# Kernel tuning notes

Measured on AMD Instinct MI355X. Metric: run time of the kernel, lower is better.

## Reference

```python
import jax, jax.numpy as jnp
import numpy as np


def setup_inputs() -> dict:
    key = jax.random.key(0)
    k1, k2, k3, k4 = jax.random.split(key, 4)
    B, C, N, K, OUT = 2, 64, 50000, 9, 64
    x = jax.random.normal(k1, (B, C, N, 1), dtype=jnp.float32)
    edge_index = jax.random.randint(k2, (2, B, N, K), 0, N, dtype=jnp.int64)
    W1 = jax.random.normal(k3, (C, C), dtype=jnp.float32) * (1.0 / np.sqrt(C))
    b1 = jnp.zeros((C,), dtype=jnp.float32)
    W2 = jax.random.normal(k4, (OUT, 2 * C), dtype=jnp.float32) * (1.0 / np.sqrt(2 * C))
    b2 = jnp.zeros((OUT,), dtype=jnp.float32)
    return {"x": x, "edge_index": edge_index, "W1": W1, "b1": b1, "W2": W2, "b2": b2}


def _gather_neighbors(x_sq, idx):
    # x_sq: [B, C, N], idx: [B, N, K] -> [B, C, N, K]
    B, C, N = x_sq.shape
    K = idx.shape[-1]
    flat = jax.vmap(lambda xb, ib: xb[:, ib])(x_sq, idx.reshape(B, N * K))
    return flat.reshape(B, C, N, K)


def reference(x, edge_index, W1, b1, W2, b2):
    # x: [B, C, N, 1]; edge_index[0]: [B, N, K] neighbor indices
    x_sq = x[..., 0]                                   # [B, C, N]
    x_j = _gather_neighbors(x_sq, edge_index[0])       # [B, C, N, K]
    # nn1: 1x1 conv (per-node linear over channels) + ReLU
    h = jax.nn.relu(jnp.einsum('bcnk,dc->bdnk', x_j, W1) + b1[None, :, None, None])
    x_j_max = jnp.max(h, axis=-1, keepdims=True)       # [B, C, N, 1]
    cat = jnp.concatenate([x, x_j_max], axis=1)        # [B, 2C, N, 1]
    # nn2: 1x1 conv + ReLU
    out = jax.nn.relu(jnp.einsum('bcnk,dc->bdnk', cat, W2) + b2[None, :, None, None])
    return out                                          # [B, OUT, N, 1]
```

## Files before the change

### kernel.cpp

```cpp
#include <hip/hip_runtime.h>
#include <cstddef>

typedef unsigned int uint;
typedef _Float16 half2v __attribute__((ext_vector_type(2)));
typedef __fp16 fp16v2 __attribute__((ext_vector_type(2)));
typedef unsigned short us2v __attribute__((ext_vector_type(2)));

union U32H2 { uint u; half2v h; fp16v2 g; us2v s; };

__device__ __forceinline__ uint pkh2(float a, float b) {
  U32H2 v; v.g = __builtin_amdgcn_cvt_pkrtz(a, b); return v.u;
}
__device__ __forceinline__ uint hmax2u(uint a, uint b) {
  U32H2 x, y, r; x.u = a; y.u = b;
  r.s = __builtin_elementwise_max(x.s, y.s);
  return r.u;
}
__device__ __forceinline__ float fdot2(uint wa, uint xa, float acc) {
  U32H2 w, x; w.u = wa; x.u = xa;
#if __has_builtin(__builtin_amdgcn_fdot2)
  return __builtin_amdgcn_fdot2(w.h, x.h, acc, false);
#else
  return acc + (float)w.h[0] * (float)x.h[0] + (float)w.h[1] * (float)x.h[1];
#endif
}

__global__ __launch_bounds__(256) void k1_node_mlp(
    const float* __restrict__ x, const float* __restrict__ W1,
    const float* __restrict__ b1, unsigned short* __restrict__ y, int N)
{
  __shared__ __align__(16) uint xs2[32 * 64];
  __shared__ __align__(16) uint wt2[32 * 64];
  const int t = threadIdx.x;
  const int nblk = (N + 63) >> 6;
  const int b = blockIdx.x / nblk;
  const int n0 = (blockIdx.x % nblk) << 6;

#pragma unroll
  for (int it = 0; it < 8; ++it) {
    const int i = t + (it << 8);
    const int n = i & 63, c2 = i >> 6;
    const bool valid = (n0 + n) < N;
    const float* xp = x + (size_t)b * 64 * N + n0 + n;
    const float a = valid ? xp[(size_t)(2 * c2) * N] : 0.0f;
    const float c = valid ? xp[(size_t)(2 * c2 + 1) * N] : 0.0f;
    xs2[c2 * 64 + n] = pkh2(a, c);
  }
#pragma unroll
  for (int it = 0; it < 8; ++it) {
    const int i = t + (it << 8);
    const int d = i & 63, c2 = i >> 6;
    wt2[c2 * 64 + d] = pkh2(W1[d * 64 + 2 * c2], W1[d * 64 + 2 * c2 + 1]);
  }
  __syncthreads();

  const int n_off = (t & 15) << 2;
  const int d0 = (t >> 4) << 2;
  float acc[4][4];
#pragma unroll
  for (int i = 0; i < 4; ++i) {
    const float bv = b1[d0 + i];
#pragma unroll
    for (int j = 0; j < 4; ++j) acc[i][j] = bv;
  }
#pragma unroll 8
  for (int c2 = 0; c2 < 32; ++c2) {
    const uint4 w = *(const uint4*)(wt2 + c2 * 64 + d0);
    const uint4 xv = *(const uint4*)(xs2 + c2 * 64 + n_off);
    const uint wa[4] = {w.x, w.y, w.z, w.w};
    const uint xa[4] = {xv.x, xv.y, xv.z, xv.w};
#pragma unroll
    for (int i = 0; i < 4; ++i)
#pragma unroll
      for (int j = 0; j < 4; ++j)
        acc[i][j] = fdot2(wa[i], xa[j], acc[i][j]);
  }
#pragma unroll
  for (int j = 0; j < 4; ++j) {
    const int n = n0 + n_off + j;
    if (n < N) {
      uint2 v;
      v.x = pkh2(fmaxf(acc[0][j], 0.f), fmaxf(acc[1][j], 0.f));
      v.y = pkh2(fmaxf(acc[2][j], 0.f), fmaxf(acc[3][j], 0.f));
      *(uint2*)(y + ((size_t)b * N + n) * 64 + d0) = v;
    }
  }
}

__global__ __launch_bounds__(256, 4) void k2_gather_out(
    const float* __restrict__ x, const int* __restrict__ eidx,
    const unsigned short* __restrict__ y, const float* __restrict__ W2,
    const float* __restrict__ b2, float* __restrict__ out, int N, int K)
{
  __shared__ __align__(16) uint ins2[64 * 64];
  __shared__ __align__(16) uint wt2[64 * 64];
  const int t = threadIdx.x;
  const int nblk = (N + 63) >> 6;
  const int b = blockIdx.x / nblk;
  const int n0 = (blockIdx.x % nblk) << 6;

  const int lane = t & 63;
  const bool is64 = (__ballot(eidx[2 * lane + 1] == 0) == ~0ull);

  const int node = lane;
  const int seg = t >> 6;
  const int n = n0 + node;
  int jj[9];
  bool act = (n < N) && (K == 9);
  if (act) {
    const size_t r = (size_t)b * N + n;
    if (is64) {
      const uint2* p = (const uint2*)(eidx + r * 18);
#pragma unroll
      for (int k = 0; k < 9; ++k) jj[k] = (int)p[k].x;
    } else {
      const int* p = eidx + r * 9;
#pragma unroll
      for (int k = 0; k < 9; ++k) jj[k] = p[k];
    }
  }

#pragma unroll
  for (int it = 0; it < 8; ++it) {
    const int i = t + (it << 8);
    const int nn = i & 63, c2 = i >> 6;
    const bool valid = (n0 + nn) < N;
    const float* xp = x + (size_t)b * 64 * N + n0 + nn;
    const float a = valid ? xp[(size_t)(2 * c2) * N] : 0.0f;
    const float c = valid ? xp[(size_t)(2 * c2 + 1) * N] : 0.0f;
    ins2[c2 * 64 + nn] = pkh2(a, c);
  }
#pragma unroll
  for (int it = 0; it < 16; ++it) {
    const int i = t + (it << 8);
    const int o = i & 63, c2 = i >> 6;
    wt2[c2 * 64 + o] = pkh2(W2[o * 128 + 2 * c2], W2[o * 128 + 2 * c2 + 1]);
  }

  uint m[8] = {0, 0, 0, 0, 0, 0, 0, 0};
  if (act) {
    const unsigned short* yb = y + (size_t)b * N * 64 + seg * 16;
    uint4 g[18];
#pragma unroll
    for (int k = 0; k < 9; ++k) {
      const uint4* yr = (const uint4*)(yb + (size_t)jj[k] * 64);
      g[2 * k] = yr[0];
      g[2 * k + 1] = yr[1];
    }
#pragma unroll
    for (int k = 0; k < 9; ++k) {
      m[0] = hmax2u(m[0], g[2 * k].x);
      m[1] = hmax2u(m[1], g[2 * k].y);
      m[2] = hmax2u(m[2], g[2 * k].z);
      m[3] = hmax2u(m[3], g[2 * k].w);
      m[4] = hmax2u(m[4], g[2 * k + 1].x);
      m[5] = hmax2u(m[5], g[2 * k + 1].y);
      m[6] = hmax2u(m[6], g[2 * k + 1].z);
      m[7] = hmax2u(m[7], g[2 * k + 1].w);
    }
  } else if (n < N) {
    const size_t r = (size_t)b * N + n;
    const unsigned short* yb = y + (size_t)b * N * 64 + seg * 16;
    for (int k = 0; k < K; ++k) {
      const int j = is64 ? (int)((const uint2*)(eidx + r * 2 * K))[k].x
                         : (eidx + r * K)[k];
      const uint4* yr = (const uint4*)(yb + (size_t)j * 64);
      const uint4 a0 = yr[0], a1 = yr[1];
      m[0] = hmax2u(m[0], a0.x); m[1] = hmax2u(m[1], a0.y);
      m[2] = hmax2u(m[2], a0.z); m[3] = hmax2u(m[3], a0.w);
      m[4] = hmax2u(m[4], a1.x); m[5] = hmax2u(m[5], a1.y);
      m[6] = hmax2u(m[6], a1.z); m[7] = hmax2u(m[7], a1.w);
    }
  }
#pragma unroll
  for (int q = 0; q < 8; ++q)
    ins2[(32 + seg * 8 + q) * 64 + node] = m[q];
  __syncthreads();

  const int n_off = (t & 15) << 2;
  const int o0 = (t >> 4) << 2;
  float acc[4][4];
#pragma unroll
  for (int i = 0; i < 4; ++i) {
    const float bv = b2[o0 + i];
#pragma unroll
    for (int j = 0; j < 4; ++j) acc[i][j] = bv;
  }
#pragma unroll 8
  for (int c2 = 0; c2 < 64; ++c2) {
    const uint4 w = *(const uint4*)(wt2 + c2 * 64 + o0);
    const uint4 xv = *(const uint4*)(ins2 + c2 * 64 + n_off);
    const uint wa[4] = {w.x, w.y, w.z, w.w};
    const uint xa[4] = {xv.x, xv.y, xv.z, xv.w};
#pragma unroll
    for (int i = 0; i < 4; ++i)
#pragma unroll
      for (int j = 0; j < 4; ++j)
        acc[i][j] = fdot2(wa[i], xa[j], acc[i][j]);
  }
#pragma unroll
  for (int i = 0; i < 4; ++i) {
    const int o = o0 + i;
    float* op = out + (size_t)(b * 64 + o) * N + n0 + n_off;
    const float4 v = make_float4(fmaxf(acc[i][0], 0.f), fmaxf(acc[i][1], 0.f),
                                 fmaxf(acc[i][2], 0.f), fmaxf(acc[i][3], 0.f));
    if (n0 + n_off + 3 < N) {
      *(float4*)op = v;
    } else {
      const float va[4] = {v.x, v.y, v.z, v.w};
      for (int j = 0; j < 4; ++j)
        if (n0 + n_off + j < N) op[j] = va[j];
    }
  }
}

extern "C" void kernel_launch(void* const* d_in, const int* in_sizes, int n_in,
                              void* d_out, int out_size, void* d_ws, size_t ws_size,
                              hipStream_t stream) {
  const float* x  = (const float*)d_in[0];
  const int*   ei = (const int*)d_in[1];
  const float* W1 = (const float*)d_in[2];
  const float* b1 = (const float*)d_in[3];
  const float* W2 = (const float*)d_in[4];
  const float* b2 = (const float*)d_in[5];
  float* out = (float*)d_out;

  const int N = in_sizes[0] / 128;
  const int K = in_sizes[1] / (4 * N);

  unsigned short* y = (unsigned short*)d_ws;

  const int nblk = (N + 63) >> 6;
  k1_node_mlp<<<2 * nblk, 256, 0, stream>>>(x, W1, b1, y, N);
  k2_gather_out<<<2 * nblk, 256, 0, stream>>>(x, ei, y, W2, b2, out, N, K);
}
```

Measured before the change: 144.9 us.

## Use MFMA 16x16x32 f16 for both node linears with node-major LDS layout

Both per-node linear layers move from scalar fdot2 register-tile GEMMs to MFMA 16x16x32 f16 instructions. Weight fragments are loaded straight from global memory into registers instead of being staged in LDS, and activations are stored node-major with padded strides. Each thread in k2 now handles one quarter of one node's channels for the neighbor max, with the 9 gathers split into batches of 5 and 4 to limit register use. Outputs are written as scalar per-channel stores, which may coalesce worse than the previous float4 stores.

```diff
diff --git a/kernel.cpp b/kernel.cpp
--- a/kernel.cpp
+++ b/kernel.cpp
@@ -2,11 +2,13 @@
 #include <cstddef>
 
 typedef unsigned int uint;
-typedef _Float16 half2v __attribute__((ext_vector_type(2)));
+typedef _Float16 v8h __attribute__((ext_vector_type(8)));
+typedef float v4f __attribute__((ext_vector_type(4)));
 typedef __fp16 fp16v2 __attribute__((ext_vector_type(2)));
 typedef unsigned short us2v __attribute__((ext_vector_type(2)));
 
-union U32H2 { uint u; half2v h; fp16v2 g; us2v s; };
+union U32H2 { uint u; fp16v2 g; us2v s; };
+union Frag8 { uint4 u4; uint u[4]; v8h h; };
 
 __device__ __forceinline__ uint pkh2(float a, float b) {
   U32H2 v; v.g = __builtin_amdgcn_cvt_pkrtz(a, b); return v.u;
@@ -16,101 +18,121 @@
   r.s = __builtin_elementwise_max(x.s, y.s);
   return r.u;
 }
-__device__ __forceinline__ float fdot2(uint wa, uint xa, float acc) {
-  U32H2 w, x; w.u = wa; x.u = xa;
-#if __has_builtin(__builtin_amdgcn_fdot2)
-  return __builtin_amdgcn_fdot2(w.h, x.h, acc, false);
-#else
-  return acc + (float)w.h[0] * (float)x.h[0] + (float)w.h[1] * (float)x.h[1];
-#endif
-}
-
-__global__ __launch_bounds__(256) void k1_node_mlp(
+
+__global__ __launch_bounds__(256, 4) void k1_node_mlp(
     const float* __restrict__ x, const float* __restrict__ W1,
-    const float* __restrict__ b1, unsigned short* __restrict__ y, int N)
+    const float* __restrict__ b1, uint* __restrict__ y, int N)
 {
-  __shared__ __align__(16) uint xs2[32 * 64];
-  __shared__ __align__(16) uint wt2[32 * 64];
+  __shared__ __align__(16) uint xlds[64 * 36];
+  __shared__ __align__(16) uint ylds[64 * 34];
   const int t = threadIdx.x;
   const int nblk = (N + 63) >> 6;
   const int b = blockIdx.x / nblk;
   const int n0 = (blockIdx.x % nblk) << 6;
-
-#pragma unroll
-  for (int it = 0; it < 8; ++it) {
-    const int i = t + (it << 8);
-    const int n = i & 63, c2 = i >> 6;
-    const bool valid = (n0 + n) < N;
-    const float* xp = x + (size_t)b * 64 * N + n0 + n;
-    const float a = valid ? xp[(size_t)(2 * c2) * N] : 0.0f;
-    const float c = valid ? xp[(size_t)(2 * c2 + 1) * N] : 0.0f;
-    xs2[c2 * 64 + n] = pkh2(a, c);
-  }
-#pragma unroll
-  for (int it = 0; it < 8; ++it) {
-    const int i = t + (it << 8);
-    const int d = i & 63, c2 = i >> 6;
-    wt2[c2 * 64 + d] = pkh2(W1[d * 64 + 2 * c2], W1[d * 64 + 2 * c2 + 1]);
+  const int lane = t & 63;
+  const int w = t >> 6;
+  const int node = t >> 2;
+  const int cg = t & 3;
+
+  {
+    const bool valid = (n0 + node) < N;
+    const float* xp = x + (size_t)b * 64 * N + n0 + node;
+    float xv[16];
+#pragma unroll
+    for (int i = 0; i < 16; ++i)
+      xv[i] = valid ? xp[(size_t)(cg * 16 + i) * N] : 0.0f;
+    uint4 p0, p1;
+    p0.x = pkh2(xv[0], xv[1]);   p0.y = pkh2(xv[2], xv[3]);
+    p0.z = pkh2(xv[4], xv[5]);   p0.w = pkh2(xv[6], xv[7]);
+    p1.x = pkh2(xv[8], xv[9]);   p1.y = pkh2(xv[10], xv[11]);
+    p1.z = pkh2(xv[12], xv[13]); p1.w = pkh2(xv[14], xv[15]);
+    uint* dst = xlds + node * 36 + cg * 8;
+    *(uint4*)dst = p0;
+    *(uint4*)(dst + 4) = p1;
+  }
+
+  Frag8 af[2];
+  {
+    const int d_row = w * 16 + (lane & 15);
+    const int kb = (lane >> 4) * 8;
+    const float* wp = W1 + d_row * 64 + kb;
+#pragma unroll
+    for (int kk = 0; kk < 2; ++kk) {
+      const float4 fa = *(const float4*)(wp + kk * 32);
+      const float4 fb = *(const float4*)(wp + kk * 32 + 4);
+      af[kk].u4.x = pkh2(fa.x, fa.y);
+      af[kk].u4.y = pkh2(fa.z, fa.w);
+      af[kk].u4.z = pkh2(fb.x, fb.y);
+      af[kk].u4.w = pkh2(fb.z, fb.w);
+    }
   }
   __syncthreads();
 
-  const int n_off = (t & 15) << 2;
-  const int d0 = (t >> 4) << 2;
-  float acc[4][4];
-#pragma unroll
-  for (int i = 0; i < 4; ++i) {
-    const float bv = b1[d0 + i];
-#pragma unroll
-    for (int j = 0; j < 4; ++j) acc[i][j] = bv;
-  }
-#pragma unroll 8
-  for (int c2 = 0; c2 < 32; ++c2) {
-    const uint4 w = *(const uint4*)(wt2 + c2 * 64 + d0);
-    const uint4 xv = *(const uint4*)(xs2 + c2 * 64 + n_off);
-    const uint wa[4] = {w.x, w.y, w.z, w.w};
-    const uint xa[4] = {xv.x, xv.y, xv.z, xv.w};
-#pragma unroll
-    for (int i = 0; i < 4; ++i)
-#pragma unroll
-      for (int j = 0; j < 4; ++j)
-        acc[i][j] = fdot2(wa[i], xa[j], acc[i][j]);
-  }
-#pragma unroll
-  for (int j = 0; j < 4; ++j) {
-    const int n = n0 + n_off + j;
-    if (n < N) {
-      uint2 v;
-      v.x = pkh2(fmaxf(acc[0][j], 0.f), fmaxf(acc[1][j], 0.f));
-      v.y = pkh2(fmaxf(acc[2][j], 0.f), fmaxf(acc[3][j], 0.f));
-      *(uint2*)(y + ((size_t)b * N + n) * 64 + d0) = v;
+  const int q = lane >> 4;
+  const int cidx = lane & 15;
+  const int d0 = w * 16;
+  v4f acc[4];
+  {
+    v4f bi;
+#pragma unroll
+    for (int r = 0; r < 4; ++r) bi[r] = b1[d0 + q * 4 + r];
+#pragma unroll
+    for (int nt = 0; nt < 4; ++nt) acc[nt] = bi;
+  }
+#pragma unroll
+  for (int nt = 0; nt < 4; ++nt) {
+#pragma unroll
+    for (int kk = 0; kk < 2; ++kk) {
+      Frag8 bf;
+      bf.u4 = *(const uint4*)(xlds + (nt * 16 + cidx) * 36 + kk * 16 + q * 4);
+      acc[nt] = __builtin_amdgcn_mfma_f32_16x16x32_f16(af[kk].h, bf.h, acc[nt], 0, 0, 0);
+    }
+  }
+
+#pragma unroll
+  for (int nt = 0; nt < 4; ++nt) {
+    const int nn = nt * 16 + cidx;
+    const uint p01 = pkh2(fmaxf(acc[nt][0], 0.f), fmaxf(acc[nt][1], 0.f));
+    const uint p23 = pkh2(fmaxf(acc[nt][2], 0.f), fmaxf(acc[nt][3], 0.f));
+    ylds[nn * 34 + (d0 >> 1) + 2 * q] = p01;
+    ylds[nn * 34 + (d0 >> 1) + 2 * q + 1] = p23;
+  }
+  __syncthreads();
+#pragma unroll
+  for (int p = 0; p < 4; ++p) {
+    const int f = t + (p << 8);
+    const int nn = f >> 4, ch = f & 15;
+    if (n0 + nn < N) {
+      const uint2 v = *(const uint2*)(ylds + nn * 34 + ch * 2);
+      *(uint2*)(y + ((size_t)b * N + n0 + nn) * 32 + ch * 2) = v;
     }
   }
 }
 
 __global__ __launch_bounds__(256, 4) void k2_gather_out(
     const float* __restrict__ x, const int* __restrict__ eidx,
-    const unsigned short* __restrict__ y, const float* __restrict__ W2,
+    const uint* __restrict__ y, const float* __restrict__ W2,
     const float* __restrict__ b2, float* __restrict__ out, int N, int K)
 {
-  __shared__ __align__(16) uint ins2[64 * 64];
-  __shared__ __align__(16) uint wt2[64 * 64];
+  __shared__ __align__(16) uint blds[64 * 68];
   const int t = threadIdx.x;
   const int nblk = (N + 63) >> 6;
   const int b = blockIdx.x / nblk;
   const int n0 = (blockIdx.x % nblk) << 6;
-
   const int lane = t & 63;
+  const int w = t >> 6;
+  const int node = t >> 2;
+  const int cg = t & 3;
+  const int n = n0 + node;
+
   const bool is64 = (__ballot(eidx[2 * lane + 1] == 0) == ~0ull);
 
-  const int node = lane;
-  const int seg = t >> 6;
-  const int n = n0 + node;
   int jj[9];
-  bool act = (n < N) && (K == 9);
+  const bool act = (n < N) && (K == 9);
   if (act) {
     const size_t r = (size_t)b * N + n;
     if (is64) {
-      const uint2* p = (const uint2*)(eidx + r * 18);
+      const uint2* p = (const uint2*)eidx + r * 9;
 #pragma unroll
       for (int k = 0; k < 9; ++k) jj[k] = (int)p[k].x;
     } else {
@@ -120,96 +142,122 @@
     }
   }
 
-#pragma unroll
-  for (int it = 0; it < 8; ++it) {
-    const int i = t + (it << 8);
-    const int nn = i & 63, c2 = i >> 6;
-    const bool valid = (n0 + nn) < N;
-    const float* xp = x + (size_t)b * 64 * N + n0 + nn;
-    const float a = valid ? xp[(size_t)(2 * c2) * N] : 0.0f;
-    const float c = valid ? xp[(size_t)(2 * c2 + 1) * N] : 0.0f;
-    ins2[c2 * 64 + nn] = pkh2(a, c);
-  }
-#pragma unroll
-  for (int it = 0; it < 16; ++it) {
-    const int i = t + (it << 8);
-    const int o = i & 63, c2 = i >> 6;
-    wt2[c2 * 64 + o] = pkh2(W2[o * 128 + 2 * c2], W2[o * 128 + 2 * c2 + 1]);
+  {
+    const bool valid = n < N;
+    const float* xp = x + (size_t)b * 64 * N + n0 + node;
+    float xv[16];
+#pragma unroll
+    for (int i = 0; i < 16; ++i)
+      xv[i] = valid ? xp[(size_t)(cg * 16 + i) * N] : 0.0f;
+    uint4 p0, p1;
+    p0.x = pkh2(xv[0], xv[1]);   p0.y = pkh2(xv[2], xv[3]);
+    p0.z = pkh2(xv[4], xv[5]);   p0.w = pkh2(xv[6], xv[7]);
+    p1.x = pkh2(xv[8], xv[9]);   p1.y = pkh2(xv[10], xv[11]);
+    p1.z = pkh2(xv[12], xv[13]); p1.w = pkh2(xv[14], xv[15]);
+    uint* dst = blds + node * 68 + cg * 8;
+    *(uint4*)dst = p0;
+    *(uint4*)(dst + 4) = p1;
+  }
+
+  Frag8 af[4];
+  {
+    const int o_row = w * 16 + (lane & 15);
+    const int kb = (lane >> 4) * 8;
+    const float* wp = W2 + o_row * 128 + kb;
+#pragma unroll
+    for (int kk = 0; kk < 4; ++kk) {
+      const float4 fa = *(const float4*)(wp + kk * 32);
+      const float4 fb = *(const float4*)(wp + kk * 32 + 4);
+      af[kk].u4.x = pkh2(fa.x, fa.y);
+      af[kk].u4.y = pkh2(fa.z, fa.w);
+      af[kk].u4.z = pkh2(fb.x, fb.y);
+      af[kk].u4.w = pkh2(fb.z, fb.w);
+    }
   }
 
   uint m[8] = {0, 0, 0, 0, 0, 0, 0, 0};
   if (act) {
-    const unsigned short* yb = y + (size_t)b * N * 64 + seg * 16;
-    uint4 g[18];
-#pragma unroll
-    for (int k = 0; k < 9; ++k) {
-      const uint4* yr = (const uint4*)(yb + (size_t)jj[k] * 64);
-      g[2 * k] = yr[0];
-      g[2 * k + 1] = yr[1];
-    }
-#pragma unroll
-    for (int k = 0; k < 9; ++k) {
-      m[0] = hmax2u(m[0], g[2 * k].x);
-      m[1] = hmax2u(m[1], g[2 * k].y);
-      m[2] = hmax2u(m[2], g[2 * k].z);
-      m[3] = hmax2u(m[3], g[2 * k].w);
-      m[4] = hmax2u(m[4], g[2 * k + 1].x);
-      m[5] = hmax2u(m[5], g[2 * k + 1].y);
-      m[6] = hmax2u(m[6], g[2 * k + 1].z);
-      m[7] = hmax2u(m[7], g[2 * k + 1].w);
+    const uint* yb = y + (size_t)b * N * 32 + cg * 8;
+    uint4 g[10];
+#pragma unroll
+    for (int k = 0; k < 5; ++k) {
+      const uint* base = yb + (size_t)jj[k] * 32;
+      g[2 * k] = *(const uint4*)base;
+      g[2 * k + 1] = *(const uint4*)(base + 4);
+    }
+#pragma unroll
+    for (int k = 0; k < 5; ++k) {
+      m[0] = hmax2u(m[0], g[2 * k].x); m[1] = hmax2u(m[1], g[2 * k].y);
+      m[2] = hmax2u(m[2], g[2 * k].z); m[3] = hmax2u(m[3], g[2 * k].w);
+      m[4] = hmax2u(m[4], g[2 * k + 1].x); m[5] = hmax2u(m[5], g[2 * k + 1].y);
+      m[6] = hmax2u(m[6], g[2 * k + 1].z); m[7] = hmax2u(m[7], g[2 * k + 1].w);
+    }
+#pragma unroll
+    for (int k = 0; k < 4; ++k) {
+      const uint* base = yb + (size_t)jj[5 + k] * 32;
+      g[2 * k] = *(const uint4*)base;
+      g[2 * k + 1] = *(const uint4*)(base + 4);
+    }
+#pragma unroll
+    for (int k = 0; k < 4; ++k) {
+      m[0] = hmax2u(m[0], g[2 * k].x); m[1] = hmax2u(m[1], g[2 * k].y);
+      m[2] = hmax2u(m[2], g[2 * k].z); m[3] = hmax2u(m[3], g[2 * k].w);
+      m[4] = hmax2u(m[4], g[2 * k + 1].x); m[5] = hmax2u(m[5], g[2 * k + 1].y);
+      m[6] = hmax2u(m[6], g[2 * k + 1].z); m[7] = hmax2u(m[7], g[2 * k + 1].w);
     }
   } else if (n < N) {
     const size_t r = (size_t)b * N + n;
-    const unsigned short* yb = y + (size_t)b * N * 64 + seg * 16;
+    const uint* yb = y + (size_t)b * N * 32 + cg * 8;
     for (int k = 0; k < K; ++k) {
-      const int j = is64 ? (int)((const uint2*)(eidx + r * 2 * K))[k].x
+      const int j = is64 ? (int)((const uint2*)eidx + r * K)[k].x
                          : (eidx + r * K)[k];
-      const uint4* yr = (const uint4*)(yb + (size_t)j * 64);
-      const uint4 a0 = yr[0], a1 = yr[1];
+      const uint* base = yb + (size_t)j * 32;
+      const uint4 a0 = *(const uint4*)base, a1 = *(const uint4*)(base + 4);
       m[0] = hmax2u(m[0], a0.x); m[1] = hmax2u(m[1], a0.y);
       m[2] = hmax2u(m[2], a0.z); m[3] = hmax2u(m[3], a0.w);
       m[4] = hmax2u(m[4], a1.x); m[5] = hmax2u(m[5], a1.y);
       m[6] = hmax2u(m[6], a1.z); m[7] = hmax2u(m[7], a1.w);
     }
   }
-#pragma unroll
-  for (int q = 0; q < 8; ++q)
-    ins2[(32 + seg * 8 + q) * 64 + node] = m[q];
+  {
+    uint* dst = blds + node * 68 + 32 + cg * 8;
+    uint4 v0; v0.x = m[0]; v0.y = m[1]; v0.z = m[2]; v0.w = m[3];
+    uint4 v1; v1.x = m[4]; v1.y = m[5]; v1.z = m[6]; v1.w = m[7];
+    *(uint4*)dst = v0;
+    *(uint4*)(dst + 4) = v1;
+  }
   __syncthreads();
 
-  const int n_off = (t & 15) << 2;
-  const int o0 = (t >> 4) << 2;
-  float acc[4][4];
-#pragma unroll
-  for (int i = 0; i < 4; ++i) {
-    const float bv = b2[o0 + i];
-#pragma unroll
-    for (int j = 0; j < 4; ++j) acc[i][j] = bv;
-  }
-#pragma unroll 8
-  for (int c2 = 0; c2 < 64; ++c2) {
-    const uint4 w = *(const uint4*)(wt2 + c2 * 64 + o0);
-    const uint4 xv = *(const uint4*)(ins2 + c2 * 64 + n_off);
-    const uint wa[4] = {w.x, w.y, w.z, w.w};
-    const uint xa[4] = {xv.x, xv.y, xv.z, xv.w};
-#pragma unroll
-    for (int i = 0; i < 4; ++i)
-#pragma unroll
-      for (int j = 0; j < 4; ++j)
-        acc[i][j] = fdot2(wa[i], xa[j], acc[i][j]);
-  }
-#pragma unroll
-  for (int i = 0; i < 4; ++i) {
-    const int o = o0 + i;
-    float* op = out + (size_t)(b * 64 + o) * N + n0 + n_off;
-    const float4 v = make_float4(fmaxf(acc[i][0], 0.f), fmaxf(acc[i][1], 0.f),
-                                 fmaxf(acc[i][2], 0.f), fmaxf(acc[i][3], 0.f));
-    if (n0 + n_off + 3 < N) {
-      *(float4*)op = v;
-    } else {
-      const float va[4] = {v.x, v.y, v.z, v.w};
-      for (int j = 0; j < 4; ++j)
-        if (n0 + n_off + j < N) op[j] = va[j];
+  const int q = lane >> 4;
+  const int cidx = lane & 15;
+  const int o0 = w * 16;
+  v4f acc[4];
+  {
+    v4f bi;
+#pragma unroll
+    for (int r = 0; r < 4; ++r) bi[r] = b2[o0 + q * 4 + r];
+#pragma unroll
+    for (int nt = 0; nt < 4; ++nt) acc[nt] = bi;
+  }
+#pragma unroll
+  for (int nt = 0; nt < 4; ++nt) {
+#pragma unroll
+    for (int kk = 0; kk < 4; ++kk) {
+      Frag8 bf;
+      bf.u4 = *(const uint4*)(blds + (nt * 16 + cidx) * 68 + kk * 16 + q * 4);
+      acc[nt] = __builtin_amdgcn_mfma_f32_16x16x32_f16(af[kk].h, bf.h, acc[nt], 0, 0, 0);
+    }
+  }
+
+#pragma unroll
+  for (int nt = 0; nt < 4; ++nt) {
+    const int nn = n0 + nt * 16 + cidx;
+    if (nn < N) {
+#pragma unroll
+      for (int r = 0; r < 4; ++r) {
+        const int o = o0 + q * 4 + r;
+        out[(size_t)(b * 64 + o) * N + nn] = fmaxf(acc[nt][r], 0.f);
+      }
     }
   }
 }
@@ -228,7 +276,7 @@
   const int N = in_sizes[0] / 128;
   const int K = in_sizes[1] / (4 * N);
 
-  unsigned short* y = (unsigned short*)d_ws;
+  uint* y = (uint*)d_ws;
 
   const int nblk = (N + 63) >> 6;
   k1_node_mlp<<<2 * nblk, 256, 0, stream>>>(x, W1, b1, y, N);
```

New measurement: 116.9 us. -19.3%, faster.
